# Kernel tuning notes

Measured on AMD Instinct MI355X. Metric: run time of the kernel, lower is better.

Reference implementation:

```python
import jax, jax.numpy as jnp
import numpy as np

THRESH = 0.5  # original code thresholds raw span logit channel 0 at 0.5


def setup_inputs() -> dict:
    key = jax.random.key(0)
    ks = jax.random.split(key, 9)
    B, S, H, P = 4, 256, 768, 54  # P = num_spo_patterns + 1
    scale = 0.02
    return {
        "sequence_output": jax.random.normal(ks[0], (B, S, H), jnp.float32),
        "W1s": jax.random.normal(ks[1], (H, H), jnp.float32) * scale,
        "b1s": jnp.zeros((H,), jnp.float32),
        "W2s": jax.random.normal(ks[2], (2, H), jnp.float32) * scale,
        "b2s": jnp.zeros((2,), jnp.float32),
        "Wp1": jax.random.normal(ks[3], (H, 2 * H), jnp.float32) * scale,
        "bp1": jnp.zeros((H,), jnp.float32),
        "Wp2": jax.random.normal(ks[4], (P, H), jnp.float32) * scale,
        "bp2": jnp.zeros((P,), jnp.float32),
    }


def reference(sequence_output, W1s, b1s, W2s, b2s, Wp1, bp1, Wp2, bp2):
    x = sequence_output                                # [B,S,H]
    B, S, H = x.shape
    # span classifier: Linear -> ReLU -> Linear
    h = jax.nn.relu(jnp.einsum('bsh,kh->bsk', x, W1s) + b1s)
    span_logits = jnp.einsum('bsh,kh->bsk', h, W2s) + b2s   # [B,S,2]
    cand = span_logits[..., 0] > THRESH                      # [B,S] candidates
    # spo pattern classifier on concat pairs: Linear(2H,H) splits into two H->H maps
    Wa, Wb = Wp1[:, :H], Wp1[:, H:]                          # subject / object halves
    ha = jnp.einsum('bsh,kh->bsk', x, Wa)                    # [B,S,H]
    hb = jnp.einsum('bsh,kh->bsk', x, Wb)                    # [B,S,H]
    pair_hidden = jax.nn.relu(ha[:, :, None, :] + hb[:, None, :, :] + bp1)  # [B,S,S,H]
    pair_logits = jnp.einsum('bijh,ph->bijp', pair_hidden, Wp2) + bp2       # [B,S,S,P]
    # valid pairs: both are candidates and subj != obj (diagonal excluded)
    not_diag = ~jnp.eye(S, dtype=bool)
    valid = cand[:, :, None] & cand[:, None, :] & not_diag   # [B,S,S]
    # dense masked equivalent of the per-pair Python loop (invalid pairs zeroed,
    # matching the zeros fallback for empty candidate sets)
    spo_pattern_logits = jnp.where(valid[..., None], pair_logits, 0.0)
    return spo_pattern_logits
```

## Files before the change

### kernel.cpp

```cpp
#include <hip/hip_runtime.h>
#include <hip/hip_bf16.h>


#define M_ROWS 1024
#define HDIM 768
#define PDIM 54
#define MAXC 256
#define KSPLIT 4
#define KSEG (HDIM / KSPLIT)
#define HKCH 8

#define CANDCNT_OFF  0
#define HA_OFF       4096
#define HB_OFF       (4096 + 786432)
#define ZERO_BYTES   (4096 + 2 * 786432)
#define CANDIDX_OFF  1576960
#define CANDSLOT_OFF 1577984
#define HPART_OFF    1582080

__global__ __launch_bounds__(256) void gemm_k_kernel(
    const float* __restrict__ x, const float* __restrict__ W1,
    float* __restrict__ hpart)
{
    __shared__ float As[2][16][68];
    __shared__ float Bs[2][16][68];

    const int m0 = blockIdx.x * 64;
    const int n0 = blockIdx.y * 64;
    const int kb = blockIdx.z * KSEG;
    const int t  = threadIdx.x;
    const int tm = t & 15;
    const int tn = t >> 4;
    const int r  = t >> 2;
    const int c4 = (t & 3) * 4;

    const float* xp = x  + (size_t)(m0 + r) * HDIM + kb + c4;
    const float* wp = W1 + (size_t)(n0 + r) * HDIM + kb + c4;

    float acc[4][4] = {};

    float4 av = *(const float4*)xp;
    float4 bv = *(const float4*)wp;
    As[0][c4+0][r] = av.x; As[0][c4+1][r] = av.y; As[0][c4+2][r] = av.z; As[0][c4+3][r] = av.w;
    Bs[0][c4+0][r] = bv.x; Bs[0][c4+1][r] = bv.y; Bs[0][c4+2][r] = bv.z; Bs[0][c4+3][r] = bv.w;
    __syncthreads();

    int buf = 0;
    for (int it = 0; it < KSEG / 16; ++it) {
        if (it < KSEG / 16 - 1) {
            av = *(const float4*)(xp + (it + 1) * 16);
            bv = *(const float4*)(wp + (it + 1) * 16);
        }
        #pragma unroll
        for (int kk = 0; kk < 16; ++kk) {
            float a[4], b[4];
            *(float4*)a = *(const float4*)&As[buf][kk][tm * 4];
            *(float4*)b = *(const float4*)&Bs[buf][kk][tn * 4];
            #pragma unroll
            for (int i = 0; i < 4; ++i)
                #pragma unroll
                for (int j = 0; j < 4; ++j)
                    acc[i][j] += a[i] * b[j];
        }
        if (it < KSEG / 16 - 1) {
            int nb = buf ^ 1;
            As[nb][c4+0][r] = av.x; As[nb][c4+1][r] = av.y; As[nb][c4+2][r] = av.z; As[nb][c4+3][r] = av.w;
            Bs[nb][c4+0][r] = bv.x; Bs[nb][c4+1][r] = bv.y; Bs[nb][c4+2][r] = bv.z; Bs[nb][c4+3][r] = bv.w;
            buf = nb;
        }
        __syncthreads();
    }

    float* dst = hpart + (size_t)blockIdx.z * (M_ROWS * HDIM);
    #pragma unroll
    for (int i = 0; i < 4; ++i) {
        float4 v = make_float4(acc[i][0], acc[i][1], acc[i][2], acc[i][3]);
        *(float4*)(dst + (size_t)(m0 + tm * 4 + i) * HDIM + n0 + tn * 4) = v;
    }
}

__global__ __launch_bounds__(256) void span_cand_kernel(
    const float* __restrict__ hpart, const float* __restrict__ b1,
    const float* __restrict__ w2row, const float* __restrict__ b2,
    int* __restrict__ candCount, int* __restrict__ candIdx,
    int* __restrict__ candSlot)
{
    const int m = blockIdx.x;
    const int t = threadIdx.x;
    float p = 0.f;
    for (int n = t; n < HDIM; n += 256) {
        float v = hpart[(size_t)m * HDIM + n]
                + hpart[(size_t)(M_ROWS * HDIM) + (size_t)m * HDIM + n]
                + hpart[(size_t)(2 * M_ROWS * HDIM) + (size_t)m * HDIM + n]
                + hpart[(size_t)(3 * M_ROWS * HDIM) + (size_t)m * HDIM + n];
        v += b1[n];
        v = v > 0.f ? v : 0.f;
        p += v * w2row[n];
    }
    __shared__ float wred[4];
    #pragma unroll
    for (int off = 32; off > 0; off >>= 1) p += __shfl_down(p, off, 64);
    if ((t & 63) == 0) wred[t >> 6] = p;
    __syncthreads();
    if (t == 0) {
        float s = wred[0] + wred[1] + wred[2] + wred[3] + b2[0];
        if (s > 0.5f) {
            int sl = atomicAdd(candCount, 1);
            if (sl < MAXC) { candIdx[sl] = m; candSlot[m] = sl; }
            else candSlot[m] = -1;
        } else {
            candSlot[m] = -1;
        }
    }
}

__global__ __launch_bounds__(256) void hab_kernel(
    const float* __restrict__ x, const float* __restrict__ Wp1,
    const int* __restrict__ candCount, const int* __restrict__ candIdx,
    float* __restrict__ ha, float* __restrict__ hb)
{
    int nc = *candCount; if (nc > MAXC) nc = MAXC;
    const int kc   = blockIdx.x >> 1;
    const int hseg = blockIdx.x & 1;
    const int kk   = threadIdx.x >> 5;
    const int lane = threadIdx.x & 31;
    const int k    = kc * HKCH + kk;
    const int hs   = hseg * 384;

    const float* wra = Wp1 + (size_t)k * (2 * HDIM) + hs;
    const float* wrb = wra + HDIM;
    float4 wa0 = *(const float4*)(wra + lane * 4);
    float4 wa1 = *(const float4*)(wra + 128 + lane * 4);
    float4 wa2 = *(const float4*)(wra + 256 + lane * 4);
    float4 wb0 = *(const float4*)(wrb + lane * 4);
    float4 wb1 = *(const float4*)(wrb + 128 + lane * 4);
    float4 wb2 = *(const float4*)(wrb + 256 + lane * 4);

    for (int slot = 0; slot < nc; ++slot) {
        int row = candIdx[slot];
        const float* xr = x + (size_t)row * HDIM + hs;
        float4 x0 = *(const float4*)(xr + lane * 4);
        float4 x1 = *(const float4*)(xr + 128 + lane * 4);
        float4 x2 = *(const float4*)(xr + 256 + lane * 4);
        float sa = wa0.x*x0.x + wa0.y*x0.y + wa0.z*x0.z + wa0.w*x0.w
                 + wa1.x*x1.x + wa1.y*x1.y + wa1.z*x1.z + wa1.w*x1.w
                 + wa2.x*x2.x + wa2.y*x2.y + wa2.z*x2.z + wa2.w*x2.w;
        float sb = wb0.x*x0.x + wb0.y*x0.y + wb0.z*x0.z + wb0.w*x0.w
                 + wb1.x*x1.x + wb1.y*x1.y + wb1.z*x1.z + wb1.w*x1.w
                 + wb2.x*x2.x + wb2.y*x2.y + wb2.z*x2.z + wb2.w*x2.w;
        #pragma unroll
        for (int off = 16; off > 0; off >>= 1) {
            sa += __shfl_down(sa, off, 32);
            sb += __shfl_down(sb, off, 32);
        }
        if (lane == 0) {
            atomicAdd(&ha[(size_t)slot * HDIM + k], sa);
            atomicAdd(&hb[(size_t)slot * HDIM + k], sb);
        }
    }
}

__global__ __launch_bounds__(256) void pair_kernel(
    const float* __restrict__ ha, const float* __restrict__ hb,
    const float* __restrict__ bp1, const float* __restrict__ Wp2,
    const float* __restrict__ bp2, const int* __restrict__ candSlot,
    float* __restrict__ out)
{
    __shared__ int plist[512];
    __shared__ int pcnt;
    __shared__ float v[HDIM];
    __shared__ float red[4][PDIM + 2];
    const int t = threadIdx.x;
    if (t == 0) pcnt = 0;
    __syncthreads();

    #pragma unroll
    for (int q = 0; q < 2; ++q) {
        int idx = blockIdx.x * 512 + q * 256 + t;
        int b = idx >> 16;
        int i = (idx >> 8) & 255;
        int j = idx & 255;
        if (i != j && candSlot[b * 256 + i] >= 0 && candSlot[b * 256 + j] >= 0) {
            int p = atomicAdd(&pcnt, 1);
            plist[p] = idx;
        }
    }
    __syncthreads();
    const int np = pcnt;

    for (int p = 0; p < np; ++p) {
        int idx = plist[p];
        int b = idx >> 16;
        int i = (idx >> 8) & 255;
        int j = idx & 255;
        int si = candSlot[b * 256 + i];
        int sj = candSlot[b * 256 + j];
        if (t < 192) {
            float4 a4 = *(const float4*)(ha + (size_t)si * HDIM + t * 4);
            float4 b4 = *(const float4*)(hb + (size_t)sj * HDIM + t * 4);
            float4 c4 = *(const float4*)(bp1 + t * 4);
            float4 r;
            r.x = a4.x + b4.x + c4.x; r.x = r.x > 0.f ? r.x : 0.f;
            r.y = a4.y + b4.y + c4.y; r.y = r.y > 0.f ? r.y : 0.f;
            r.z = a4.z + b4.z + c4.z; r.z = r.z > 0.f ? r.z : 0.f;
            r.w = a4.w + b4.w + c4.w; r.w = r.w > 0.f ? r.w : 0.f;
            *(float4*)(v + t * 4) = r;
        }
        __syncthreads();
        if (t < 216) {
            int pp  = t % PDIM;
            int seg = t / PDIM;
            const float* w  = Wp2 + (size_t)pp * HDIM + seg * 192;
            const float* vv = v + seg * 192;
            float s = 0.f;
            for (int h = 0; h < 192; h += 4) {
                float4 a  = *(const float4*)(vv + h);
                float4 b2 = *(const float4*)(w + h);
                s += a.x * b2.x + a.y * b2.y + a.z * b2.z + a.w * b2.w;
            }
            red[seg][pp] = s;
        }
        __syncthreads();
        if (t < PDIM)
            out[(size_t)idx * PDIM + t] = red[0][t] + red[1][t] + red[2][t] + red[3][t] + bp2[t];
        __syncthreads();
    }
}

extern "C" void kernel_launch(void* const* d_in, const int* in_sizes, int n_in,
                              void* d_out, int out_size, void* d_ws, size_t ws_size,
                              hipStream_t stream) {
    const float* x   = (const float*)d_in[0];
    const float* W1s = (const float*)d_in[1];
    const float* b1s = (const float*)d_in[2];
    const float* W2s = (const float*)d_in[3];
    const float* b2s = (const float*)d_in[4];
    const float* Wp1 = (const float*)d_in[5];
    const float* bp1 = (const float*)d_in[6];
    const float* Wp2 = (const float*)d_in[7];
    const float* bp2 = (const float*)d_in[8];

    char* ws = (char*)d_ws;
    int*   candCnt  = (int*)(ws + CANDCNT_OFF);
    float* ha       = (float*)(ws + HA_OFF);
    float* hb       = (float*)(ws + HB_OFF);
    int*   candIdx  = (int*)(ws + CANDIDX_OFF);
    int*   candSlot = (int*)(ws + CANDSLOT_OFF);
    float* hpart    = (float*)(ws + HPART_OFF);
    float* out = (float*)d_out;

    hipMemsetAsync(out, 0, (size_t)out_size * sizeof(float), stream);
    hipMemsetAsync(ws, 0, ZERO_BYTES, stream);

    dim3 g(M_ROWS / 64, HDIM / 64, KSPLIT);
    gemm_k_kernel<<<g, 256, 0, stream>>>(x, W1s, hpart);

    span_cand_kernel<<<M_ROWS, 256, 0, stream>>>(hpart, b1s, W2s, b2s,
                                                 candCnt, candIdx, candSlot);

    hab_kernel<<<192, 256, 0, stream>>>(x, Wp1, candCnt, candIdx, ha, hb);

    pair_kernel<<<512, 256, 0, stream>>>(ha, hb, bp1, Wp2, bp2, candSlot, out);
}
```

Measured before the change: 151.2 us.

## Remove memsets by fusing zeroing into kernels and dropping hab atomics

Drops both hipMemsetAsync calls. The output is now zeroed inside pair_kernel, and the candidate counter is reset inside gemm_k_kernel. hab_kernel now has each warp cover the full hidden dimension, so it writes ha/hb directly instead of using atomicAdd, and it launches half as many blocks. The GEMM also loses its register-prefetch double buffering in favour of a simpler single-buffer loop, which trades load/compute overlap for less shared memory and fewer registers.

```diff
diff --git a/kernel.cpp b/kernel.cpp
--- a/kernel.cpp
+++ b/kernel.cpp
@@ -8,22 +8,23 @@
 #define MAXC 256
 #define KSPLIT 4
 #define KSEG (HDIM / KSPLIT)
-#define HKCH 8
 
 #define CANDCNT_OFF  0
-#define HA_OFF       4096
-#define HB_OFF       (4096 + 786432)
-#define ZERO_BYTES   (4096 + 2 * 786432)
-#define CANDIDX_OFF  1576960
-#define CANDSLOT_OFF 1577984
-#define HPART_OFF    1582080
+#define CANDIDX_OFF  1024
+#define CANDSLOT_OFF 8192
+#define HA_OFF       16384
+#define HB_OFF       (16384 + 786432)
+#define HPART_OFF    (16384 + 2 * 786432)
 
 __global__ __launch_bounds__(256) void gemm_k_kernel(
     const float* __restrict__ x, const float* __restrict__ W1,
-    float* __restrict__ hpart)
-{
-    __shared__ float As[2][16][68];
-    __shared__ float Bs[2][16][68];
+    float* __restrict__ hpart, int* __restrict__ candCnt)
+{
+    __shared__ float As[16][68];
+    __shared__ float Bs[16][68];
+
+    if (threadIdx.x == 0 && blockIdx.x == 0 && blockIdx.y == 0 && blockIdx.z == 0)
+        *candCnt = 0;
 
     const int m0 = blockIdx.x * 64;
     const int n0 = blockIdx.y * 64;
@@ -34,39 +35,24 @@
     const int r  = t >> 2;
     const int c4 = (t & 3) * 4;
 
-    const float* xp = x  + (size_t)(m0 + r) * HDIM + kb + c4;
-    const float* wp = W1 + (size_t)(n0 + r) * HDIM + kb + c4;
-
     float acc[4][4] = {};
 
-    float4 av = *(const float4*)xp;
-    float4 bv = *(const float4*)wp;
-    As[0][c4+0][r] = av.x; As[0][c4+1][r] = av.y; As[0][c4+2][r] = av.z; As[0][c4+3][r] = av.w;
-    Bs[0][c4+0][r] = bv.x; Bs[0][c4+1][r] = bv.y; Bs[0][c4+2][r] = bv.z; Bs[0][c4+3][r] = bv.w;
-    __syncthreads();
-
-    int buf = 0;
-    for (int it = 0; it < KSEG / 16; ++it) {
-        if (it < KSEG / 16 - 1) {
-            av = *(const float4*)(xp + (it + 1) * 16);
-            bv = *(const float4*)(wp + (it + 1) * 16);
-        }
+    for (int k0 = kb; k0 < kb + KSEG; k0 += 16) {
+        float4 av = *(const float4*)(x  + (size_t)(m0 + r) * HDIM + k0 + c4);
+        float4 bv = *(const float4*)(W1 + (size_t)(n0 + r) * HDIM + k0 + c4);
+        As[c4+0][r] = av.x; As[c4+1][r] = av.y; As[c4+2][r] = av.z; As[c4+3][r] = av.w;
+        Bs[c4+0][r] = bv.x; Bs[c4+1][r] = bv.y; Bs[c4+2][r] = bv.z; Bs[c4+3][r] = bv.w;
+        __syncthreads();
         #pragma unroll
         for (int kk = 0; kk < 16; ++kk) {
             float a[4], b[4];
-            *(float4*)a = *(const float4*)&As[buf][kk][tm * 4];
-            *(float4*)b = *(const float4*)&Bs[buf][kk][tn * 4];
+            *(float4*)a = *(const float4*)&As[kk][tm * 4];
+            *(float4*)b = *(const float4*)&Bs[kk][tn * 4];
             #pragma unroll
             for (int i = 0; i < 4; ++i)
                 #pragma unroll
                 for (int j = 0; j < 4; ++j)
                     acc[i][j] += a[i] * b[j];
-        }
-        if (it < KSEG / 16 - 1) {
-            int nb = buf ^ 1;
-            As[nb][c4+0][r] = av.x; As[nb][c4+1][r] = av.y; As[nb][c4+2][r] = av.z; As[nb][c4+3][r] = av.w;
-            Bs[nb][c4+0][r] = bv.x; Bs[nb][c4+1][r] = bv.y; Bs[nb][c4+2][r] = bv.z; Bs[nb][c4+3][r] = bv.w;
-            buf = nb;
         }
         __syncthreads();
     }
@@ -120,42 +106,36 @@
     float* __restrict__ ha, float* __restrict__ hb)
 {
     int nc = *candCount; if (nc > MAXC) nc = MAXC;
-    const int kc   = blockIdx.x >> 1;
-    const int hseg = blockIdx.x & 1;
     const int kk   = threadIdx.x >> 5;
     const int lane = threadIdx.x & 31;
-    const int k    = kc * HKCH + kk;
-    const int hs   = hseg * 384;
-
-    const float* wra = Wp1 + (size_t)k * (2 * HDIM) + hs;
-    const float* wrb = wra + HDIM;
-    float4 wa0 = *(const float4*)(wra + lane * 4);
-    float4 wa1 = *(const float4*)(wra + 128 + lane * 4);
-    float4 wa2 = *(const float4*)(wra + 256 + lane * 4);
-    float4 wb0 = *(const float4*)(wrb + lane * 4);
-    float4 wb1 = *(const float4*)(wrb + 128 + lane * 4);
-    float4 wb2 = *(const float4*)(wrb + 256 + lane * 4);
+    const int k    = blockIdx.x * 8 + kk;
+
+    const float* wr = Wp1 + (size_t)k * (2 * HDIM);
+    float4 wa[6], wb[6];
+    #pragma unroll
+    for (int c = 0; c < 6; ++c) {
+        wa[c] = *(const float4*)(wr + c * 128 + lane * 4);
+        wb[c] = *(const float4*)(wr + HDIM + c * 128 + lane * 4);
+    }
 
     for (int slot = 0; slot < nc; ++slot) {
         int row = candIdx[slot];
-        const float* xr = x + (size_t)row * HDIM + hs;
-        float4 x0 = *(const float4*)(xr + lane * 4);
-        float4 x1 = *(const float4*)(xr + 128 + lane * 4);
-        float4 x2 = *(const float4*)(xr + 256 + lane * 4);
-        float sa = wa0.x*x0.x + wa0.y*x0.y + wa0.z*x0.z + wa0.w*x0.w
-                 + wa1.x*x1.x + wa1.y*x1.y + wa1.z*x1.z + wa1.w*x1.w
-                 + wa2.x*x2.x + wa2.y*x2.y + wa2.z*x2.z + wa2.w*x2.w;
-        float sb = wb0.x*x0.x + wb0.y*x0.y + wb0.z*x0.z + wb0.w*x0.w
-                 + wb1.x*x1.x + wb1.y*x1.y + wb1.z*x1.z + wb1.w*x1.w
-                 + wb2.x*x2.x + wb2.y*x2.y + wb2.z*x2.z + wb2.w*x2.w;
+        const float* xr = x + (size_t)row * HDIM;
+        float sa = 0.f, sb = 0.f;
+        #pragma unroll
+        for (int c = 0; c < 6; ++c) {
+            float4 xv = *(const float4*)(xr + c * 128 + lane * 4);
+            sa += wa[c].x*xv.x + wa[c].y*xv.y + wa[c].z*xv.z + wa[c].w*xv.w;
+            sb += wb[c].x*xv.x + wb[c].y*xv.y + wb[c].z*xv.z + wb[c].w*xv.w;
+        }
         #pragma unroll
         for (int off = 16; off > 0; off >>= 1) {
             sa += __shfl_down(sa, off, 32);
             sb += __shfl_down(sb, off, 32);
         }
         if (lane == 0) {
-            atomicAdd(&ha[(size_t)slot * HDIM + k], sa);
-            atomicAdd(&hb[(size_t)slot * HDIM + k], sb);
+            ha[(size_t)slot * HDIM + k] = sa;
+            hb[(size_t)slot * HDIM + k] = sb;
         }
     }
 }
@@ -171,6 +151,13 @@
     __shared__ float v[HDIM];
     __shared__ float red[4][PDIM + 2];
     const int t = threadIdx.x;
+
+    float* outb = out + (size_t)blockIdx.x * 512 * PDIM;
+    float4 z = make_float4(0.f, 0.f, 0.f, 0.f);
+    #pragma unroll
+    for (int q = 0; q < 27; ++q)
+        *(float4*)(outb + (size_t)(q * 256 + t) * 4) = z;
+
     if (t == 0) pcnt = 0;
     __syncthreads();
 
@@ -242,23 +229,20 @@
 
     char* ws = (char*)d_ws;
     int*   candCnt  = (int*)(ws + CANDCNT_OFF);
+    int*   candIdx  = (int*)(ws + CANDIDX_OFF);
+    int*   candSlot = (int*)(ws + CANDSLOT_OFF);
     float* ha       = (float*)(ws + HA_OFF);
     float* hb       = (float*)(ws + HB_OFF);
-    int*   candIdx  = (int*)(ws + CANDIDX_OFF);
-    int*   candSlot = (int*)(ws + CANDSLOT_OFF);
     float* hpart    = (float*)(ws + HPART_OFF);
     float* out = (float*)d_out;
 
-    hipMemsetAsync(out, 0, (size_t)out_size * sizeof(float), stream);
-    hipMemsetAsync(ws, 0, ZERO_BYTES, stream);
-
     dim3 g(M_ROWS / 64, HDIM / 64, KSPLIT);
-    gemm_k_kernel<<<g, 256, 0, stream>>>(x, W1s, hpart);
+    gemm_k_kernel<<<g, 256, 0, stream>>>(x, W1s, hpart, candCnt);
 
     span_cand_kernel<<<M_ROWS, 256, 0, stream>>>(hpart, b1s, W2s, b2s,
                                                  candCnt, candIdx, candSlot);
 
-    hab_kernel<<<192, 256, 0, stream>>>(x, Wp1, candCnt, candIdx, ha, hb);
+    hab_kernel<<<96, 256, 0, stream>>>(x, Wp1, candCnt, candIdx, ha, hb);
 
     pair_kernel<<<512, 256, 0, stream>>>(ha, hb, bp1, Wp2, bp2, candSlot, out);
 }
```

Result: faster. 147.4 us (-2.5%).
